# Optimization experiments

Hardware: AMD Instinct MI355X
Metric: run time of the kernel (lower is better)

The kernel has to match this reference:

```python
import jax, jax.numpy as jnp
import numpy as np
from jax import lax

B, T, D = 2, 512, 64   # batch, temporal length, input_dim
H = 64                 # hidden_dims
OUT = 64               # output_dim
REL = 2 * D            # relation_dim = input_dim * 2 (until=True: max & min interval pooling)


def _interval_pool(f, op):
    """f: [B,T,D] -> r: [B,T,T,D] with r[:, i, j] = op-reduction of f[:, i..j] for i <= j.
    Entries with i > j are filled with f[:, i] (degenerate interval); they are never
    read because the downstream backward pooling only reduces over j >= i."""
    Tn = f.shape[1]
    idx = jnp.arange(Tn)

    def step(col, j):
        # col[:, i] holds reduce(f[:, i..j-1]) for i <= j-1, and f[:, i] otherwise
        new = op(col, f[:, j][:, None, :])                      # extend interval to j
        new = jnp.where((idx <= j)[None, :, None], new, f)      # reset i > j rows
        return new, new

    _, cols = lax.scan(step, f, jnp.arange(Tn))  # [T(j), B, T(i), D]
    return jnp.transpose(cols, (1, 2, 0, 3))     # [B, T(i), T(j), D]


def _backward_max_pool(s):
    """s: [B,T,T,C] -> out[:, i] = max_{j >= i} s[:, i, j]  (the 'broadcast' backward pool)."""
    Tn = s.shape[1]
    mask = jnp.arange(Tn)[:, None] <= jnp.arange(Tn)[None, :]   # i <= j
    neg = jnp.asarray(-1e9, s.dtype)
    return jnp.max(jnp.where(mask[None, :, :, None], s, neg), axis=2)


def setup_inputs() -> dict:
    key = jax.random.key(0)
    ks = jax.random.split(key, 7)
    f = jax.random.normal(ks[0], (B, T, D), dtype=jnp.float32)
    # step_linears per __init__: current_dim starts at REL, then hidden_dims
    dims = [(REL + REL, H), (H + REL, H), (H + REL, OUT)]
    params = {}
    for i, (din, dout) in enumerate(dims):
        params[f"W{i}"] = jax.random.normal(ks[1 + 2 * i], (din, dout), jnp.float32) / np.sqrt(din)
        params[f"b{i}"] = jnp.zeros((dout,), jnp.float32)
    return {"f": f, **params}


def reference(f, W0, b0, W1, b1, W2, b2):
    Tn = f.shape[1]
    # until=True: concat max- and min-interval pooling -> [B,T,T,2D]
    r = jnp.concatenate([_interval_pool(f, jnp.maximum),
                         _interval_pool(f, jnp.minimum)], axis=-1)
    current = r[:, :, Tn - 1]  # [B, T, REL] : reductions over suffix intervals [i, T-1]
    for W, b in ((W0, b0), (W1, b1), (W2, b2)):
        # jactorch.add_dim(current, 1, t): broadcast current (indexed by j) over new i axis
        bcast = jnp.broadcast_to(current[:, None, :, :],
                                 (f.shape[0], Tn, Tn, current.shape[-1]))
        li = jnp.concatenate([bcast, r], axis=-1)                 # [B,T,T,C+REL]
        h = jax.nn.sigmoid(jnp.einsum('bijc,co->bijo', li, W) + b)  # MLPLogic, no hidden layers
        current = _backward_max_pool(h)                           # [B,T,out]
    return current
```

## Files before the change

kernel.cpp:

```cpp
#include <hip/hip_runtime.h>
#include <hip/hip_bf16.h>
#include <math.h>

#define B_ 2
#define T_ 512
#define D_ 64
#define NBLK8_PER_B 544

typedef __attribute__((ext_vector_type(8))) short bf16x8;
typedef __attribute__((ext_vector_type(8))) unsigned short u16x8;
typedef __attribute__((ext_vector_type(4))) float f32x4;

static __device__ __forceinline__ unsigned short f2bf(float v) {
    __hip_bfloat16 h = __float2bfloat16(v);
    return *reinterpret_cast<unsigned short*>(&h);
}
static __device__ __forceinline__ float bf2f(unsigned short u) {
    return __uint_as_float(((unsigned)u) << 16);
}
static __device__ __forceinline__ unsigned short maxbits(unsigned short a, unsigned short b) {
    float m = fmaxf(bf2f(a), bf2f(b));
    return (unsigned short)(__float_as_uint(m) >> 16);
}
static __device__ __forceinline__ unsigned short minbits(unsigned short a, unsigned short b) {
    float m = fminf(bf2f(a), bf2f(b));
    return (unsigned short)(__float_as_uint(m) >> 16);
}

__global__ __launch_bounds__(512) void prep_kernel(
    const float* __restrict__ f,
    const float* __restrict__ W0, const float* __restrict__ W1, const float* __restrict__ W2,
    unsigned short* __restrict__ tmax, unsigned short* __restrict__ tmin,
    unsigned short* __restrict__ wf,
    unsigned short* __restrict__ cur0bf, unsigned short* __restrict__ intra,
    float* __restrict__ z0, float* __restrict__ z1, float* __restrict__ z2) {

    __shared__ unsigned short lmax[512][16];
    __shared__ unsigned short lmin[512][16];

    const int blk = blockIdx.x;
    const int tid = threadIdx.x;

    if (blk < 8) {
        const int b = blk & 1;
        const int c0 = (blk >> 1) * 16;
        const int t = tid;

        u16x8 mx[2], mn[2];
#pragma unroll
        for (int h = 0; h < 2; ++h) {
            const float* fp = &f[((size_t)(b * T_ + t) << 6) + c0 + h * 8];
#pragma unroll
            for (int e = 0; e < 8; ++e) {
                unsigned short u = f2bf(fp[e]);
                mx[h][e] = u; mn[h][e] = u;
            }
            size_t base = ((size_t)(b * T_ + t) << 6) + c0 + h * 8;
            *reinterpret_cast<u16x8*>(&tmax[base]) = mx[h];
            *reinterpret_cast<u16x8*>(&tmin[base]) = mn[h];
        }
        for (int k = 1; k <= 9; ++k) {
            *reinterpret_cast<u16x8*>(&lmax[t][0]) = mx[0];
            *reinterpret_cast<u16x8*>(&lmax[t][8]) = mx[1];
            *reinterpret_cast<u16x8*>(&lmin[t][0]) = mn[0];
            *reinterpret_cast<u16x8*>(&lmin[t][8]) = mn[1];
            __syncthreads();
            int t2 = t + (1 << (k - 1));
            if (t2 > T_ - 1) t2 = T_ - 1;
            u16x8 qx0 = *reinterpret_cast<const u16x8*>(&lmax[t2][0]);
            u16x8 qx1 = *reinterpret_cast<const u16x8*>(&lmax[t2][8]);
            u16x8 qn0 = *reinterpret_cast<const u16x8*>(&lmin[t2][0]);
            u16x8 qn1 = *reinterpret_cast<const u16x8*>(&lmin[t2][8]);
#pragma unroll
            for (int e = 0; e < 8; ++e) {
                mx[0][e] = maxbits(mx[0][e], qx0[e]);
                mx[1][e] = maxbits(mx[1][e], qx1[e]);
                mn[0][e] = minbits(mn[0][e], qn0[e]);
                mn[1][e] = minbits(mn[1][e], qn1[e]);
            }
            size_t base = ((size_t)((k * B_ + b) * T_ + t) << 6) + c0;
            *reinterpret_cast<u16x8*>(&tmax[base]) = mx[0];
            *reinterpret_cast<u16x8*>(&tmax[base + 8]) = mx[1];
            *reinterpret_cast<u16x8*>(&tmin[base]) = mn[0];
            *reinterpret_cast<u16x8*>(&tmin[base + 8]) = mn[1];
            __syncthreads();
        }
    } else if (blk < 11) {
        const int layer = blk - 8;
        const float* W = (layer == 0) ? W0 : ((layer == 1) ? W1 : W2);
        const int FRS = (layer == 0) ? 32 : 24;
        const int l = tid & 63;
        for (int fr = tid >> 6; fr < FRS; fr += 8) {
            int kt = fr >> 2, nt = fr & 3;
#pragma unroll
            for (int e = 0; e < 8; ++e) {
                int row = kt * 32 + ((l >> 4) << 3) + e;
                int col = nt * 16 + (l & 15);
                wf[((size_t)(layer * 32 + fr) * 64 + l) * 8 + e] = f2bf(W[row * 64 + col]);
            }
        }
    } else if (blk < 139) {
        const int x = blk - 11;
        const int c = x & 63, b = x >> 6;
        const int t = tid;
        float* smax = reinterpret_cast<float*>(lmax);
        float* smin = reinterpret_cast<float*>(lmin);
        float v = f[((size_t)(b * T_ + t) << 6) + c];
        smax[t] = v; smin[t] = v;
        __syncthreads();
        for (int off = 1; off < 512; off <<= 1) {
            float a = (t + off < 512) ? smax[t + off] : -1e30f;
            float m = (t + off < 512) ? smin[t + off] : 1e30f;
            __syncthreads();
            smax[t] = fmaxf(smax[t], a);
            smin[t] = fminf(smin[t], m);
            __syncthreads();
        }
        cur0bf[((size_t)(b * T_ + t) << 7) + c] = f2bf(smax[t]);
        cur0bf[((size_t)(b * T_ + t) << 7) + 64 + c] = f2bf(smin[t]);
    } else if (blk < 171) {
        const int x = blk - 139;
        const int jt = x & 15, b = x >> 4;
        const int jj = tid >> 4, c8 = tid & 15;
        const bool ismin = c8 >= 8;
        unsigned short (*sc)[128] = reinterpret_cast<unsigned short (*)[128]>(lmax);

        const float* fp = &f[((size_t)(b * T_ + jt * 32 + jj) << 6) + (c8 & 7) * 8];
        u16x8 r;
#pragma unroll
        for (int e = 0; e < 8; ++e) r[e] = f2bf(fp[e]);

#pragma unroll
        for (int off = 1; off < 32; off <<= 1) {
            *reinterpret_cast<u16x8*>(&sc[jj][c8 * 8]) = r;
            __syncthreads();
            if (jj >= off) {
                u16x8 q = *reinterpret_cast<const u16x8*>(&sc[jj - off][c8 * 8]);
#pragma unroll
                for (int e = 0; e < 8; ++e)
                    r[e] = ismin ? minbits(r[e], q[e]) : maxbits(r[e], q[e]);
            }
            __syncthreads();
        }
        *reinterpret_cast<u16x8*>(&intra[((size_t)((b * 16 + jt) * 32 + jj) << 7) + c8 * 8]) = r;
    } else {
        int fi = (blk - 171) * 512 + tid;
        float4 z = {0.f, 0.f, 0.f, 0.f};
        if (fi < 16384)       reinterpret_cast<float4*>(z0)[fi] = z;
        else if (fi < 32768)  reinterpret_cast<float4*>(z1)[fi - 16384] = z;
        else                  reinterpret_cast<float4*>(z2)[fi - 32768] = z;
    }
}

template <int C, bool FROM_TAB>
__global__ __launch_bounds__(512) void pair_kernel(
    const unsigned short* __restrict__ tabmax,
    const unsigned short* __restrict__ tabmin,
    const unsigned short* __restrict__ cur0bf,
    const unsigned short* __restrict__ intra,
    const float* __restrict__ curprev,
    const unsigned short* __restrict__ wf,
    const float* __restrict__ bias,
    float* __restrict__ out) {

    constexpr int KTC = C / 32;
    constexpr int KT = KTC + 4;
    constexpr int CP = (C == 128) ? 136 : 72;

    int m = blockIdx.x;
    int b = 0;
    if (m >= NBLK8_PER_B) { b = 1; m -= NBLK8_PER_B; }
    int jt, it;
    bool diag;
    if (m < 64) {
        diag = true;
        jt = m >> 2;
        it = 4 * jt + (m & 3);
    } else {
        diag = false;
        int m2 = m - 64;
        jt = 1;
        while (m2 >= 2 * jt * (jt + 1)) ++jt;
        it = m2 - 2 * jt * (jt - 1);
    }
    const int i0 = it * 8, j0 = jt * 32;

    const int tid = threadIdx.x;
    const int l = tid & 63, w = tid >> 6;
    const int lg = l >> 4, li = l & 15;
    const int pi = i0 + w;

    __shared__ unsigned short curl[32][CP];
    __shared__ unsigned short intr[32][136];
    __shared__ unsigned short pref[8][136];
    __shared__ unsigned short wlds[KT * 4 * 64 * 8];

#pragma unroll
    for (int q = 0; q < KT / 2; ++q) {
        int idx = q * 512 + tid;
        u16x8 v = *reinterpret_cast<const u16x8*>(&wf[(size_t)idx * 8]);
        *reinterpret_cast<u16x8*>(&wlds[idx * 8]) = v;
    }

    if (FROM_TAB) {
        int jj = tid >> 4, c8 = tid & 15;
        u16x8 v = *reinterpret_cast<const u16x8*>(
            &cur0bf[((size_t)(b * T_ + j0 + jj) << 7) + c8 * 8]);
        *reinterpret_cast<u16x8*>(&curl[jj][c8 * 8]) = v;
    } else if (tid < 256) {
        int jj = tid >> 3, c8 = tid & 7;
        const float* cp = &curprev[((size_t)(b * T_ + j0 + jj) << 6) + c8 * 8];
        float4 v0 = *reinterpret_cast<const float4*>(cp);
        float4 v1 = *reinterpret_cast<const float4*>(cp + 4);
        u16x8 r;
        r[0] = f2bf(v0.x); r[1] = f2bf(v0.y); r[2] = f2bf(v0.z); r[3] = f2bf(v0.w);
        r[4] = f2bf(v1.x); r[5] = f2bf(v1.y); r[6] = f2bf(v1.z); r[7] = f2bf(v1.w);
        *reinterpret_cast<u16x8*>(&curl[jj][c8 * 8]) = r;
    }

    if (!diag) {
        {
            int jj = tid >> 4, c8 = tid & 15;
            u16x8 v = *reinterpret_cast<const u16x8*>(
                &intra[((size_t)((b * 16 + jt) * 32 + jj) << 7) + c8 * 8]);
            *reinterpret_cast<u16x8*>(&intr[jj][c8 * 8]) = v;
        }
        if (tid < 128) {
            int isel = tid >> 4, c8 = tid & 15;
            int i = i0 + isel;
            int len = j0 - i;
            int kk = 31 - __clz(len);
            int t2 = j0 - (1 << kk);
            const unsigned short* tab = (c8 < 8) ? tabmax : tabmin;
            int cc = (c8 & 7) * 8;
            u16x8 va = *reinterpret_cast<const u16x8*>(&tab[(((size_t)(kk * B_ + b) * T_ + i) << 6) + cc]);
            u16x8 vb = *reinterpret_cast<const u16x8*>(&tab[(((size_t)(kk * B_ + b) * T_ + t2) << 6) + cc]);
            u16x8 r;
#pragma unroll
            for (int e = 0; e < 8; ++e)
                r[e] = (c8 < 8) ? maxbits(va[e], vb[e]) : minbits(va[e], vb[e]);
            *reinterpret_cast<u16x8*>(&pref[isel][c8 * 8]) = r;
        }
    }
    __syncthreads();

    int kk_q[2], t2_q[2];
    if (diag) {
#pragma unroll
        for (int s = 0; s < 2; ++s) {
            int pj = j0 + 16 * s + li;
            int je = (pj < pi) ? pi : pj;
            int len = je - pi + 1;
            kk_q[s] = 31 - __clz(len);
            t2_q[s] = je + 1 - (1 << kk_q[s]);
        }
    }

    f32x4 acc[2][4];
#pragma unroll
    for (int s = 0; s < 2; ++s)
#pragma unroll
        for (int nt = 0; nt < 4; ++nt) acc[s][nt] = (f32x4){0.f, 0.f, 0.f, 0.f};

#pragma unroll
    for (int kt = 0; kt < KT; ++kt) {
        bf16x8 wfr[4];
#pragma unroll
        for (int nt = 0; nt < 4; ++nt)
            wfr[nt] = *reinterpret_cast<const bf16x8*>(&wlds[((kt * 4 + nt) * 64 + l) * 8]);

#pragma unroll
        for (int s = 0; s < 2; ++s) {
            const int pjj = 16 * s + li;
            bf16x8 av;
            if (kt < KTC) {
                av = *reinterpret_cast<const bf16x8*>(&curl[pjj][kt * 32 + lg * 8]);
            } else {
                const int krt = kt - KTC;
                if (!diag) {
                    u16x8 iv = *reinterpret_cast<const u16x8*>(&intr[pjj][(krt * 4 + lg) * 8]);
                    u16x8 pv = *reinterpret_cast<const u16x8*>(&pref[w][(krt * 4 + lg) * 8]);
                    if (krt < 2) {
#pragma unroll
                        for (int e = 0; e < 8; ++e) av[e] = (short)maxbits(iv[e], pv[e]);
                    } else {
#pragma unroll
                        for (int e = 0; e < 8; ++e) av[e] = (short)minbits(iv[e], pv[e]);
                    }
                } else {
                    const int c8 = krt * 4 + lg;
                    const unsigned short* tab = (krt < 2) ? tabmax : tabmin;
                    const int cc = (c8 & 7) * 8;
                    const int kku = kk_q[s], t2u = t2_q[s];
                    u16x8 va = *reinterpret_cast<const u16x8*>(&tab[(((size_t)(kku * B_ + b) * T_ + pi) << 6) + cc]);
                    u16x8 vb = *reinterpret_cast<const u16x8*>(&tab[(((size_t)(kku * B_ + b) * T_ + t2u) << 6) + cc]);
                    if (krt < 2) {
#pragma unroll
                        for (int e = 0; e < 8; ++e) av[e] = (short)maxbits(va[e], vb[e]);
                    } else {
#pragma unroll
                        for (int e = 0; e < 8; ++e) av[e] = (short)minbits(va[e], vb[e]);
                    }
                }
            }
#pragma unroll
            for (int nt = 0; nt < 4; ++nt)
                acc[s][nt] = __builtin_amdgcn_mfma_f32_16x16x32_bf16(av, wfr[nt], acc[s][nt], 0, 0, 0);
        }
    }

#pragma unroll
    for (int nt = 0; nt < 4; ++nt) {
        float vm = -1e9f;
#pragma unroll
        for (int s = 0; s < 2; ++s)
#pragma unroll
            for (int r = 0; r < 4; ++r) {
                int jj = 16 * s + lg * 4 + r;
                if (!diag || (j0 + jj >= pi)) vm = fmaxf(vm, acc[s][nt][r]);
            }
        vm = fmaxf(vm, __shfl_xor(vm, 16));
        vm = fmaxf(vm, __shfl_xor(vm, 32));
        if (l < 16) {
            int o = nt * 16 + li;
            float h = 1.0f / (1.0f + __expf(-(vm + bias[o])));
            atomicMax((int*)out + (((size_t)(b * T_ + pi) << 6) + o), __float_as_int(h));
        }
    }
}

extern "C" void kernel_launch(void* const* d_in, const int* in_sizes, int n_in,
                              void* d_out, int out_size, void* d_ws, size_t ws_size,
                              hipStream_t stream) {
    const float* f  = (const float*)d_in[0];
    const float* W0 = (const float*)d_in[1];
    const float* b0 = (const float*)d_in[2];
    const float* W1 = (const float*)d_in[3];
    const float* b1 = (const float*)d_in[4];
    const float* W2 = (const float*)d_in[5];
    const float* b2 = (const float*)d_in[6];
    float* outp = (float*)d_out;

    unsigned short* tabmax = (unsigned short*)d_ws;
    unsigned short* tabmin = tabmax + 10 * B_ * T_ * 64;
    unsigned short* wf     = tabmin + 10 * B_ * T_ * 64;
    unsigned short* cur0bf = wf + 3 * 32 * 64 * 8;
    unsigned short* intra  = cur0bf + B_ * T_ * 128;
    float* cur1 = (float*)(intra + B_ * 16 * 32 * 128);
    float* cur2 = cur1 + B_ * T_ * 64;

    prep_kernel<<<dim3(267), dim3(512), 0, stream>>>(f, W0, W1, W2,
                                                     tabmax, tabmin, wf,
                                                     cur0bf, intra,
                                                     cur1, cur2, outp);

    const dim3 pgrid(B_ * NBLK8_PER_B);
    pair_kernel<128, true ><<<pgrid, dim3(512), 0, stream>>>(tabmax, tabmin, cur0bf, intra,
                                                             nullptr, wf + 0 * 32 * 64 * 8, b0, cur1);
    pair_kernel<64,  false><<<pgrid, dim3(512), 0, stream>>>(tabmax, tabmin, cur0bf, intra,
                                                             cur1, wf + 1 * 32 * 64 * 8, b1, cur2);
    pair_kernel<64,  false><<<pgrid, dim3(512), 0, stream>>>(tabmax, tabmin, cur0bf, intra,
                                                             cur2, wf + 2 * 32 * 64 * 8, b2, outp);
}
```

Baseline: 78.23 us.

## Factor the broadcast-current matmul into a per-j precomputed term outside the pair kernel

The linear layer on the concatenated input is split into W_top·current[j] + W_bot·r[i,j]. The current-dependent part, plus bias, is computed once per (b,j) by small new g0/g64 kernels and added in the epilogue. Each pair block now runs only the four relation K-tiles of MFMA instead of KTC+4, which removes redundant work repeated across every i. The costs are three extra small kernel launches, the block ordering now interleaving batches, and the current term now summed in fp32 rather than bf16 MFMA.

Result: no change. 77.59 us (-0.8%).

```diff
diff --git a/kernel.cpp b/kernel.cpp
--- a/kernel.cpp
+++ b/kernel.cpp
@@ -5,7 +5,6 @@
 #define B_ 2
 #define T_ 512
 #define D_ 64
-#define NBLK8_PER_B 544
 
 typedef __attribute__((ext_vector_type(8))) short bf16x8;
 typedef __attribute__((ext_vector_type(8))) unsigned short u16x8;
@@ -32,7 +31,7 @@
     const float* __restrict__ W0, const float* __restrict__ W1, const float* __restrict__ W2,
     unsigned short* __restrict__ tmax, unsigned short* __restrict__ tmin,
     unsigned short* __restrict__ wf,
-    unsigned short* __restrict__ cur0bf, unsigned short* __restrict__ intra,
+    unsigned short* __restrict__ intra,
     float* __restrict__ z0, float* __restrict__ z1, float* __restrict__ z2) {
 
     __shared__ unsigned short lmax[512][16];
@@ -88,38 +87,21 @@
     } else if (blk < 11) {
         const int layer = blk - 8;
         const float* W = (layer == 0) ? W0 : ((layer == 1) ? W1 : W2);
-        const int FRS = (layer == 0) ? 32 : 24;
+        const int Coff = (layer == 0) ? 128 : 64;
         const int l = tid & 63;
-        for (int fr = tid >> 6; fr < FRS; fr += 8) {
+#pragma unroll
+        for (int q = 0; q < 2; ++q) {
+            int fr = (tid >> 6) + q * 8;
             int kt = fr >> 2, nt = fr & 3;
 #pragma unroll
             for (int e = 0; e < 8; ++e) {
-                int row = kt * 32 + ((l >> 4) << 3) + e;
+                int row = Coff + kt * 32 + ((l >> 4) << 3) + e;
                 int col = nt * 16 + (l & 15);
-                wf[((size_t)(layer * 32 + fr) * 64 + l) * 8 + e] = f2bf(W[row * 64 + col]);
-            }
-        }
-    } else if (blk < 139) {
+                wf[((size_t)(layer * 16 + fr) * 64 + l) * 8 + e] = f2bf(W[row * 64 + col]);
+            }
+        }
+    } else if (blk < 43) {
         const int x = blk - 11;
-        const int c = x & 63, b = x >> 6;
-        const int t = tid;
-        float* smax = reinterpret_cast<float*>(lmax);
-        float* smin = reinterpret_cast<float*>(lmin);
-        float v = f[((size_t)(b * T_ + t) << 6) + c];
-        smax[t] = v; smin[t] = v;
-        __syncthreads();
-        for (int off = 1; off < 512; off <<= 1) {
-            float a = (t + off < 512) ? smax[t + off] : -1e30f;
-            float m = (t + off < 512) ? smin[t + off] : 1e30f;
-            __syncthreads();
-            smax[t] = fmaxf(smax[t], a);
-            smin[t] = fminf(smin[t], m);
-            __syncthreads();
-        }
-        cur0bf[((size_t)(b * T_ + t) << 7) + c] = f2bf(smax[t]);
-        cur0bf[((size_t)(b * T_ + t) << 7) + 64 + c] = f2bf(smin[t]);
-    } else if (blk < 171) {
-        const int x = blk - 139;
         const int jt = x & 15, b = x >> 4;
         const int jj = tid >> 4, c8 = tid & 15;
         const bool ismin = c8 >= 8;
@@ -144,7 +126,7 @@
         }
         *reinterpret_cast<u16x8*>(&intra[((size_t)((b * 16 + jt) * 32 + jj) << 7) + c8 * 8]) = r;
     } else {
-        int fi = (blk - 171) * 512 + tid;
+        int fi = (blk - 43) * 512 + tid;
         float4 z = {0.f, 0.f, 0.f, 0.f};
         if (fi < 16384)       reinterpret_cast<float4*>(z0)[fi] = z;
         else if (fi < 32768)  reinterpret_cast<float4*>(z1)[fi - 16384] = z;
@@ -152,36 +134,82 @@
     }
 }
 
-template <int C, bool FROM_TAB>
+__global__ __launch_bounds__(256) void g0_kernel(
+    const unsigned short* __restrict__ tabmax,
+    const unsigned short* __restrict__ tabmin,
+    const float* __restrict__ W0, const float* __restrict__ bias,
+    float* __restrict__ g) {
+
+    __shared__ float cur_lds[4][128];
+
+    const int tid = threadIdx.x;
+    const int bt0 = blockIdx.x * 4;
+
+    if (tid < 64) {
+        int isel = tid >> 4, c8 = tid & 15;
+        int bt = bt0 + isel;
+        int b = bt >> 9, t = bt & 511;
+        int len = T_ - t;
+        int kk = 31 - __clz(len);
+        int t2 = T_ - (1 << kk);
+        const unsigned short* tab = (c8 < 8) ? tabmax : tabmin;
+        int cc = (c8 & 7) * 8;
+        u16x8 va = *reinterpret_cast<const u16x8*>(&tab[(((size_t)(kk * B_ + b) * T_ + t) << 6) + cc]);
+        u16x8 vb = *reinterpret_cast<const u16x8*>(&tab[(((size_t)(kk * B_ + b) * T_ + t2) << 6) + cc]);
+#pragma unroll
+        for (int e = 0; e < 8; ++e) {
+            unsigned short r = (c8 < 8) ? maxbits(va[e], vb[e]) : minbits(va[e], vb[e]);
+            cur_lds[isel][c8 * 8 + e] = bf2f(r);
+        }
+    }
+    __syncthreads();
+
+    const int r = tid >> 6, o = tid & 63;
+    float s = bias[o];
+#pragma unroll 8
+    for (int c = 0; c < 128; ++c)
+        s = fmaf(cur_lds[r][c], W0[c * 64 + o], s);
+    g[((size_t)(bt0 + r) << 6) + o] = s;
+}
+
+__global__ __launch_bounds__(256) void g64_kernel(
+    const float* __restrict__ cur, const float* __restrict__ W,
+    const float* __restrict__ bias, float* __restrict__ g) {
+    const int bt = blockIdx.x * 4 + (threadIdx.x >> 6);
+    const int o = threadIdx.x & 63;
+    float s = bias[o];
+    const float* cp = &cur[(size_t)bt << 6];
+#pragma unroll 8
+    for (int c = 0; c < 64; ++c)
+        s = fmaf(cp[c], W[c * 64 + o], s);
+    g[((size_t)bt << 6) + o] = s;
+}
+
 __global__ __launch_bounds__(512) void pair_kernel(
     const unsigned short* __restrict__ tabmax,
     const unsigned short* __restrict__ tabmin,
-    const unsigned short* __restrict__ cur0bf,
     const unsigned short* __restrict__ intra,
-    const float* __restrict__ curprev,
     const unsigned short* __restrict__ wf,
-    const float* __restrict__ bias,
+    const float* __restrict__ g,
     float* __restrict__ out) {
 
-    constexpr int KTC = C / 32;
-    constexpr int KT = KTC + 4;
-    constexpr int CP = (C == 128) ? 136 : 72;
-
     int m = blockIdx.x;
-    int b = 0;
-    if (m >= NBLK8_PER_B) { b = 1; m -= NBLK8_PER_B; }
-    int jt, it;
+    int b, jt, it;
     bool diag;
-    if (m < 64) {
+    if (m < 128) {
         diag = true;
-        jt = m >> 2;
-        it = 4 * jt + (m & 3);
+        b = m & 1;
+        int idx = m >> 1;
+        jt = idx >> 2;
+        it = 4 * jt + (idx & 3);
     } else {
         diag = false;
-        int m2 = m - 64;
+        int m2 = m - 128;
+        b = m2 & 1;
+        int m3 = m2 >> 1;
         jt = 1;
-        while (m2 >= 2 * jt * (jt + 1)) ++jt;
-        it = m2 - 2 * jt * (jt - 1);
+        while (m3 >= 2 * jt * (jt + 1)) ++jt;
+        it = m3 - 2 * jt * (jt - 1);
     }
     const int i0 = it * 8, j0 = jt * 32;
 
@@ -190,32 +218,22 @@
     const int lg = l >> 4, li = l & 15;
     const int pi = i0 + w;
 
-    __shared__ unsigned short curl[32][CP];
     __shared__ unsigned short intr[32][136];
     __shared__ unsigned short pref[8][136];
-    __shared__ unsigned short wlds[KT * 4 * 64 * 8];
-
-#pragma unroll
-    for (int q = 0; q < KT / 2; ++q) {
+    __shared__ unsigned short wlds[16 * 64 * 8];
+    __shared__ float gl[32][68];
+
+#pragma unroll
+    for (int q = 0; q < 2; ++q) {
         int idx = q * 512 + tid;
         u16x8 v = *reinterpret_cast<const u16x8*>(&wf[(size_t)idx * 8]);
         *reinterpret_cast<u16x8*>(&wlds[idx * 8]) = v;
     }
 
-    if (FROM_TAB) {
-        int jj = tid >> 4, c8 = tid & 15;
-        u16x8 v = *reinterpret_cast<const u16x8*>(
-            &cur0bf[((size_t)(b * T_ + j0 + jj) << 7) + c8 * 8]);
-        *reinterpret_cast<u16x8*>(&curl[jj][c8 * 8]) = v;
-    } else if (tid < 256) {
-        int jj = tid >> 3, c8 = tid & 7;
-        const float* cp = &curprev[((size_t)(b * T_ + j0 + jj) << 6) + c8 * 8];
-        float4 v0 = *reinterpret_cast<const float4*>(cp);
-        float4 v1 = *reinterpret_cast<const float4*>(cp + 4);
-        u16x8 r;
-        r[0] = f2bf(v0.x); r[1] = f2bf(v0.y); r[2] = f2bf(v0.z); r[3] = f2bf(v0.w);
-        r[4] = f2bf(v1.x); r[5] = f2bf(v1.y); r[6] = f2bf(v1.z); r[7] = f2bf(v1.w);
-        *reinterpret_cast<u16x8*>(&curl[jj][c8 * 8]) = r;
+    {
+        int jj = tid >> 4, c4 = tid & 15;
+        float4 v = *reinterpret_cast<const float4*>(&g[((size_t)(b * T_ + j0 + jj) << 6) + c4 * 4]);
+        *reinterpret_cast<float4*>(&gl[jj][c4 * 4]) = v;
     }
 
     if (!diag) {
@@ -263,44 +281,39 @@
         for (int nt = 0; nt < 4; ++nt) acc[s][nt] = (f32x4){0.f, 0.f, 0.f, 0.f};
 
 #pragma unroll
-    for (int kt = 0; kt < KT; ++kt) {
+    for (int krt = 0; krt < 4; ++krt) {
         bf16x8 wfr[4];
 #pragma unroll
         for (int nt = 0; nt < 4; ++nt)
-            wfr[nt] = *reinterpret_cast<const bf16x8*>(&wlds[((kt * 4 + nt) * 64 + l) * 8]);
+            wfr[nt] = *reinterpret_cast<const bf16x8*>(&wlds[((krt * 4 + nt) * 64 + l) * 8]);
 
 #pragma unroll
         for (int s = 0; s < 2; ++s) {
             const int pjj = 16 * s + li;
             bf16x8 av;
-            if (kt < KTC) {
-                av = *reinterpret_cast<const bf16x8*>(&curl[pjj][kt * 32 + lg * 8]);
+            if (!diag) {
+                u16x8 iv = *reinterpret_cast<const u16x8*>(&intr[pjj][(krt * 4 + lg) * 8]);
+                u16x8 pv = *reinterpret_cast<const u16x8*>(&pref[w][(krt * 4 + lg) * 8]);
+                if (krt < 2) {
+#pragma unroll
+                    for (int e = 0; e < 8; ++e) av[e] = (short)maxbits(iv[e], pv[e]);
+                } else {
+#pragma unroll
+                    for (int e = 0; e < 8; ++e) av[e] = (short)minbits(iv[e], pv[e]);
+                }
             } else {
-                const int krt = kt - KTC;
-                if (!diag) {
-                    u16x8 iv = *reinterpret_cast<const u16x8*>(&intr[pjj][(krt * 4 + lg) * 8]);
-                    u16x8 pv = *reinterpret_cast<const u16x8*>(&pref[w][(krt * 4 + lg) * 8]);
-                    if (krt < 2) {
-#pragma unroll
-                        for (int e = 0; e < 8; ++e) av[e] = (short)maxbits(iv[e], pv[e]);
-                    } else {
-#pragma unroll
-                        for (int e = 0; e < 8; ++e) av[e] = (short)minbits(iv[e], pv[e]);
-                    }
+                const int c8 = krt * 4 + lg;
+                const unsigned short* tab = (krt < 2) ? tabmax : tabmin;
+                const int cc = (c8 & 7) * 8;
+                const int kku = kk_q[s], t2u = t2_q[s];
+                u16x8 va = *reinterpret_cast<const u16x8*>(&tab[(((size_t)(kku * B_ + b) * T_ + pi) << 6) + cc]);
+                u16x8 vb = *reinterpret_cast<const u16x8*>(&tab[(((size_t)(kku * B_ + b) * T_ + t2u) << 6) + cc]);
+                if (krt < 2) {
+#pragma unroll
+                    for (int e = 0; e < 8; ++e) av[e] = (short)maxbits(va[e], vb[e]);
                 } else {
-                    const int c8 = krt * 4 + lg;
-                    const unsigned short* tab = (krt < 2) ? tabmax : tabmin;
-                    const int cc = (c8 & 7) * 8;
-                    const int kku = kk_q[s], t2u = t2_q[s];
-                    u16x8 va = *reinterpret_cast<const u16x8*>(&tab[(((size_t)(kku * B_ + b) * T_ + pi) << 6) + cc]);
-                    u16x8 vb = *reinterpret_cast<const u16x8*>(&tab[(((size_t)(kku * B_ + b) * T_ + t2u) << 6) + cc]);
-                    if (krt < 2) {
-#pragma unroll
-                        for (int e = 0; e < 8; ++e) av[e] = (short)maxbits(va[e], vb[e]);
-                    } else {
-#pragma unroll
-                        for (int e = 0; e < 8; ++e) av[e] = (short)minbits(va[e], vb[e]);
-                    }
+#pragma unroll
+                    for (int e = 0; e < 8; ++e) av[e] = (short)minbits(va[e], vb[e]);
                 }
             }
 #pragma unroll
@@ -311,19 +324,20 @@
 
 #pragma unroll
     for (int nt = 0; nt < 4; ++nt) {
+        const int o = nt * 16 + li;
         float vm = -1e9f;
 #pragma unroll
         for (int s = 0; s < 2; ++s)
 #pragma unroll
             for (int r = 0; r < 4; ++r) {
                 int jj = 16 * s + lg * 4 + r;
-                if (!diag || (j0 + jj >= pi)) vm = fmaxf(vm, acc[s][nt][r]);
+                float v = acc[s][nt][r] + gl[jj][o];
+                if (!diag || (j0 + jj >= pi)) vm = fmaxf(vm, v);
             }
         vm = fmaxf(vm, __shfl_xor(vm, 16));
         vm = fmaxf(vm, __shfl_xor(vm, 32));
         if (l < 16) {
-            int o = nt * 16 + li;
-            float h = 1.0f / (1.0f + __expf(-(vm + bias[o])));
+            float h = 1.0f / (1.0f + __expf(-vm));
             atomicMax((int*)out + (((size_t)(b * T_ + pi) << 6) + o), __float_as_int(h));
         }
     }
@@ -344,21 +358,27 @@
     unsigned short* tabmax = (unsigned short*)d_ws;
     unsigned short* tabmin = tabmax + 10 * B_ * T_ * 64;
     unsigned short* wf     = tabmin + 10 * B_ * T_ * 64;
-    unsigned short* cur0bf = wf + 3 * 32 * 64 * 8;
-    unsigned short* intra  = cur0bf + B_ * T_ * 128;
+    unsigned short* intra  = wf + 3 * 16 * 64 * 8;
     float* cur1 = (float*)(intra + B_ * 16 * 32 * 128);
     float* cur2 = cur1 + B_ * T_ * 64;
-
-    prep_kernel<<<dim3(267), dim3(512), 0, stream>>>(f, W0, W1, W2,
-                                                     tabmax, tabmin, wf,
-                                                     cur0bf, intra,
+    float* gbuf = cur2 + B_ * T_ * 64;
+
+    prep_kernel<<<dim3(139), dim3(512), 0, stream>>>(f, W0, W1, W2,
+                                                     tabmax, tabmin, wf, intra,
                                                      cur1, cur2, outp);
 
-    const dim3 pgrid(B_ * NBLK8_PER_B);
-    pair_kernel<128, true ><<<pgrid, dim3(512), 0, stream>>>(tabmax, tabmin, cur0bf, intra,
-                                                             nullptr, wf + 0 * 32 * 64 * 8, b0, cur1);
-    pair_kernel<64,  false><<<pgrid, dim3(512), 0, stream>>>(tabmax, tabmin, cur0bf, intra,
-                                                             cur1, wf + 1 * 32 * 64 * 8, b1, cur2);
-    pair_kernel<64,  false><<<pgrid, dim3(512), 0, stream>>>(tabmax, tabmin, cur0bf, intra,
-                                                             cur2, wf + 2 * 32 * 64 * 8, b2, outp);
-}
+    const dim3 pgrid(B_ * 544);
+    const dim3 ggrid(B_ * T_ / 4);
+
+    g0_kernel<<<ggrid, dim3(256), 0, stream>>>(tabmax, tabmin, W0, b0, gbuf);
+    pair_kernel<<<pgrid, dim3(512), 0, stream>>>(tabmax, tabmin, intra,
+                                                 wf + 0 * 8192, gbuf, cur1);
+
+    g64_kernel<<<ggrid, dim3(256), 0, stream>>>(cur1, W1, b1, gbuf);
+    pair_kernel<<<pgrid, dim3(512), 0, stream>>>(tabmax, tabmin, intra,
+                                                 wf + 1 * 8192, gbuf, cur2);
+
+    g64_kernel<<<ggrid, dim3(256), 0, stream>>>(cur2, W2, b2, gbuf);
+    pair_kernel<<<pgrid, dim3(512), 0, stream>>>(tabmax, tabmin, intra,
+                                                 wf + 2 * 8192, gbuf, outp);
+}
```
